# Performance work log

Measured on AMD Instinct MI355X. Metric: run time of the kernel, lower is better.

## Reference

```python
import jax, jax.numpy as jnp
import numpy as np
from jax import lax

K = 3  # kernel size
CO = 64  # out_channels
CI = 64  # in_channels


def setup_inputs() -> dict:
    key = jax.random.key(0)
    k1, k2, k3, k4, k5 = jax.random.split(key, 5)
    x = jax.random.normal(k1, (16, CI, 128, 128), dtype=jnp.float32)
    w1 = jax.random.normal(k2, (2 * CI, 32), dtype=jnp.float32) * 0.05
    b1 = jax.random.normal(k3, (32,), dtype=jnp.float32) * 0.05
    w2 = jax.random.normal(k4, (32, CO * CI * K * K), dtype=jnp.float32) * 0.05
    b2 = jax.random.normal(k5, (CO * CI * K * K,), dtype=jnp.float32) * 0.05
    return {"x": x, "w1": w1, "b1": b1, "w2": w2, "b2": b2}


def reference(x, w1, b1, w2, b2):
    B = x.shape[0]
    # per-sample channel statistics over spatial dims (torch.std is unbiased, ddof=1)
    mean = jnp.mean(x, axis=(2, 3))                      # [B, CI]
    std = jnp.std(x, axis=(2, 3), ddof=1)                # [B, CI]
    stats = jnp.concatenate([mean, std], axis=-1)        # [B, 2*CI]
    h = jax.nn.relu(stats @ w1 + b1)                     # [B, 32]
    kernels = (h @ w2 + b2).reshape(B, CO, CI, K, K)     # per-sample conv kernels

    def conv_one(xi, wi):
        # xi: [CI,H,W], wi: [CO,CI,K,K]; stride=1, padding=1, no bias
        return lax.conv_general_dilated(
            xi[None], wi, window_strides=(1, 1), padding=[(1, 1), (1, 1)],
            dimension_numbers=("NCHW", "OIHW", "NCHW"))[0]

    return jax.vmap(conv_one)(x, kernels)                # [B, CO, H, W]
```

## Files before the change

kernel.cpp:

```cpp
#include <hip/hip_runtime.h>
#include <hip/hip_bf16.h>


#define B_ 16
#define NPIX 16384
#define KEL 36864
#define XT_RS 8320

typedef __attribute__((ext_vector_type(4))) float f32x4;
typedef __attribute__((ext_vector_type(8))) short short8;

static __device__ __forceinline__ short bf16_of(float f) {
    __hip_bfloat16 h = __float2bfloat16(f);
    return *reinterpret_cast<short*>(&h);
}

__global__ __launch_bounds__(256) void xpose_stats(const float* __restrict__ x,
                                                   short* __restrict__ xT,
                                                   float* __restrict__ part) {
    int b = blockIdx.x, cig = blockIdx.y, pt = blockIdx.z;
    int t = threadIdx.x;
    int y = pt * 8 + (t >> 5);
    int x0 = (t & 31) * 4;

    const float* xb = x + ((size_t)(b * 64 + cig * 8)) * NPIX;
    short* xTb = xT + (size_t)b * 128 * XT_RS;

    float s[8], ss[8];
    f32x4 v[8];
    #pragma unroll
    for (int c = 0; c < 8; c++) {
        v[c] = *(const f32x4*)(xb + (size_t)c * NPIX + y * 128 + x0);
        s[c]  = v[c][0] + v[c][1] + v[c][2] + v[c][3];
        ss[c] = v[c][0]*v[c][0] + v[c][1]*v[c][1] + v[c][2]*v[c][2] + v[c][3]*v[c][3];
    }
    #pragma unroll
    for (int xi = 0; xi < 4; xi++) {
        short8 o;
        #pragma unroll
        for (int c = 0; c < 8; c++) o[c] = bf16_of(v[c][xi]);
        *(short8*)(xTb + ((size_t)(y * 130 + x0 + xi + 1)) * 64 + cig * 8) = o;
    }
    if (t < 16) {
        int y2 = pt * 8 + (t & 7);
        int col = (t & 8) ? 129 : 0;
        short8 z = {0, 0, 0, 0, 0, 0, 0, 0};
        *(short8*)(xTb + ((size_t)(y2 * 130 + col)) * 64 + cig * 8) = z;
    }

    __shared__ float red[4][16];
    int lane = t & 63, w = t >> 6;
    #pragma unroll
    for (int c = 0; c < 8; c++) {
        float a = s[c], q = ss[c];
        for (int off = 32; off; off >>= 1) { a += __shfl_down(a, off); q += __shfl_down(q, off); }
        if (lane == 0) { red[w][c * 2] = a; red[w][c * 2 + 1] = q; }
    }
    __syncthreads();
    if (t < 16)
        part[((size_t)((b * 8 + cig) * 16 + pt)) * 16 + t] =
            red[0][t] + red[1][t] + red[2][t] + red[3][t];
}

__global__ __launch_bounds__(256) void kern_gen(const float* __restrict__ part,
                                                const float* __restrict__ w1,
                                                const float* __restrict__ b1,
                                                const float* __restrict__ w2,
                                                const float* __restrict__ b2,
                                                short* __restrict__ wT) {
    __shared__ float st[16][128];
    __shared__ float hT[32][16];
    int t = threadIdx.x;

    for (int id = t; id < 1024; id += 256) {
        int b = id >> 6, ci = id & 63;
        const float* pb = part + ((size_t)((b * 8 + (ci >> 3)) * 16)) * 16 + (ci & 7) * 2;
        float s = 0.f, q = 0.f;
        #pragma unroll
        for (int p = 0; p < 16; p++) { s += pb[p * 16]; q += pb[p * 16 + 1]; }
        float mean = s * (1.f / NPIX);
        float var = fmaxf((q - s * mean) * (1.f / (NPIX - 1)), 0.f);
        st[b][ci] = mean;
        st[b][64 + ci] = sqrtf(var);
    }
    __syncthreads();
    for (int id = t; id < 512; id += 256) {
        int b = id >> 5, jj = id & 31;
        float acc = b1[jj];
        for (int i = 0; i < 128; i++) acc += st[b][i] * w1[i * 32 + jj];
        hT[jj][b] = fmaxf(acc, 0.f);
    }
    __syncthreads();

    int j = blockIdx.x * 256 + t;
    float wv[32];
    #pragma unroll
    for (int i = 0; i < 32; i++) wv[i] = w2[(size_t)i * KEL + j];
    float bv = b2[j];

    float acc[16];
    #pragma unroll
    for (int b = 0; b < 16; b++) acc[b] = bv;
    #pragma unroll
    for (int i = 0; i < 32; i++) {
        float wvi = wv[i];
        const f32x4* hr = (const f32x4*)&hT[i][0];
        #pragma unroll
        for (int q4 = 0; q4 < 4; q4++) {
            f32x4 hq = hr[q4];
            acc[q4 * 4 + 0] += hq[0] * wvi;
            acc[q4 * 4 + 1] += hq[1] * wvi;
            acc[q4 * 4 + 2] += hq[2] * wvi;
            acc[q4 * 4 + 3] += hq[3] * wvi;
        }
    }

    int co = j / 576;
    int rem = j - co * 576;
    int ci = rem / 9;
    int tap = rem - ci * 9;
    size_t dst = (size_t)tap * 4096 + co * 64 + ((((ci >> 3) ^ (co & 7)) << 3) | (ci & 7));
    #pragma unroll
    for (int b = 0; b < 16; b++)
        wT[(size_t)b * KEL + dst] = bf16_of(acc[b]);
}

__global__ __launch_bounds__(512, 1) void conv_mfma(const short* __restrict__ xT,
                                                    const short* __restrict__ wT,
                                                    float* __restrict__ out) {
    __shared__ __align__(16) short xls[10 * 528 * 8];
    __shared__ __align__(16) short wls[9 * 512 * 8];

    int b = blockIdx.x, xt = blockIdx.y, yo = blockIdx.z;
    int x0 = xt * 64, y0 = yo * 8;
    int t = threadIdx.x;
    int l = t & 63, w = t >> 6;
    int xq = w & 3, rh = w >> 2;
    int l15 = l & 15, lg = l >> 4;

    const short* xTb = xT + (size_t)b * 128 * XT_RS;
    const short* wTb = wT + (size_t)b * KEL;

    #pragma unroll
    for (int it = 0; it < 9; it++) {
        int e = it * 512 + t;
        __builtin_amdgcn_global_load_lds(
            (const __attribute__((address_space(1))) void*)(wTb + (size_t)e * 8),
            (__attribute__((address_space(3))) void*)(wls + (it * 512 + (t & ~63)) * 8),
            16, 0, 0);
    }
    #pragma unroll
    for (int lr = 0; lr < 10; lr++) {
        int y = y0 - 1 + lr;
        if (y < 0 || y > 127) {
            short8 z8 = {0, 0, 0, 0, 0, 0, 0, 0};
            for (int e = t; e < 528; e += 512)
                *(short8*)(xls + (lr * 528 + e) * 8) = z8;
        } else {
            #pragma unroll
            for (int it = 0; it < 2; it++) {
                int e = it * 512 + t;
                if (e < 528) {
                    int xi = e >> 3, s = e & 7;
                    const short* src = xTb + (size_t)y * XT_RS
                        + (x0 + xi) * 64 + ((s ^ (xi & 7)) << 3);
                    __builtin_amdgcn_global_load_lds(
                        (const __attribute__((address_space(1))) void*)src,
                        (__attribute__((address_space(3))) void*)
                            (xls + (lr * 528 + it * 512 + (t & ~63)) * 8),
                        16, 0, 0);
                }
            }
        }
    }
    asm volatile("s_waitcnt vmcnt(0) lgkmcnt(0)" ::: "memory");
    __builtin_amdgcn_s_barrier();
    __builtin_amdgcn_sched_barrier(0);

    f32x4 acc[4][4];
    #pragma unroll
    for (int r = 0; r < 4; r++)
        #pragma unroll
        for (int g = 0; g < 4; g++) acc[r][g] = (f32x4){0.f, 0.f, 0.f, 0.f};

    #pragma unroll
    for (int kp = 0; kp < 2; kp++) {
        int sig = kp * 4 + lg;
        int pa = sig ^ (l15 & 7);
        #pragma unroll
        for (int tap = 0; tap < 9; tap++) {
            const int dy = tap / 3, dx = tap % 3;
            short8 a[4], bf[4];
            #pragma unroll
            for (int g = 0; g < 4; g++)
                a[g] = *(const short8*)&wls[(tap * 512 + (g * 16 + l15) * 8 + pa) * 8];
            int xi = xq * 16 + l15 + dx;
            int sw = sig ^ (xi & 7);
            #pragma unroll
            for (int r = 0; r < 4; r++)
                bf[r] = *(const short8*)&xls[((rh * 4 + r + dy) * 528 + xi * 8 + sw) * 8];
            #pragma unroll
            for (int r = 0; r < 4; r++)
                #pragma unroll
                for (int g = 0; g < 4; g++)
                    acc[r][g] = __builtin_amdgcn_mfma_f32_16x16x32_bf16(a[g], bf[r], acc[r][g], 0, 0, 0);
        }
    }

    #pragma unroll
    for (int g = 0; g < 4; g++) {
        float* ob = out + ((size_t)(b * 64 + g * 16 + lg * 4)) * NPIX
                        + (y0 + rh * 4) * 128 + x0 + xq * 16 + l15;
        #pragma unroll
        for (int reg = 0; reg < 4; reg++)
            #pragma unroll
            for (int r = 0; r < 4; r++)
                ob[(size_t)reg * NPIX + r * 128] = acc[r][g][reg];
    }
}

extern "C" void kernel_launch(void* const* d_in, const int* in_sizes, int n_in,
                              void* d_out, int out_size, void* d_ws, size_t ws_size,
                              hipStream_t stream) {
    const float* x  = (const float*)d_in[0];
    const float* w1 = (const float*)d_in[1];
    const float* b1 = (const float*)d_in[2];
    const float* w2 = (const float*)d_in[3];
    const float* b2 = (const float*)d_in[4];
    float* out = (float*)d_out;

    float* part = (float*)d_ws;
    short* wT = (short*)((char*)d_ws + 131072);
    short* xT = (short*)((char*)d_ws + 131072 + 1179648);

    xpose_stats<<<dim3(B_, 8, 16), 256, 0, stream>>>(x, xT, part);
    kern_gen<<<dim3(144), 256, 0, stream>>>(part, w1, b1, w2, b2, wT);
    conv_mfma<<<dim3(B_, 2, 16), 512, 0, stream>>>(xT, wT, out);
}
```

Baseline: 66.40 us.

## Keep conv weights in registers and shrink row tile to raise occupancy

Measured after the change: 115.0 us. +73.1%, slower.

```diff
diff --git a/kernel.cpp b/kernel.cpp
--- a/kernel.cpp
+++ b/kernel.cpp
@@ -119,103 +119,111 @@
     int rem = j - co * 576;
     int ci = rem / 9;
     int tap = rem - ci * 9;
-    size_t dst = (size_t)tap * 4096 + co * 64 + ((((ci >> 3) ^ (co & 7)) << 3) | (ci & 7));
+    size_t dst = (size_t)co * 576 + tap * 64 + ci;
     #pragma unroll
     for (int b = 0; b < 16; b++)
         wT[(size_t)b * KEL + dst] = bf16_of(acc[b]);
 }
 
-__global__ __launch_bounds__(512, 1) void conv_mfma(const short* __restrict__ xT,
-                                                    const short* __restrict__ wT,
-                                                    float* __restrict__ out) {
-    __shared__ __align__(16) short xls[10 * 528 * 8];
-    __shared__ __align__(16) short wls[9 * 512 * 8];
-
-    int b = blockIdx.x, xt = blockIdx.y, yo = blockIdx.z;
-    int x0 = xt * 64, y0 = yo * 8;
+__global__ __attribute__((amdgpu_flat_work_group_size(512, 512),
+                          amdgpu_waves_per_eu(4, 4)))
+void conv_mfma(const short* __restrict__ xT,
+               const short* __restrict__ wT,
+               float* __restrict__ out) {
+    __shared__ __align__(16) short xls[6 * 528 * 8];
+
+    int b = blockIdx.x, xt = blockIdx.y, yt = blockIdx.z;
+    int x0 = xt * 64, y0 = yt * 4;
     int t = threadIdx.x;
     int l = t & 63, w = t >> 6;
-    int xq = w & 3, rh = w >> 2;
+    int cog = w & 3, rh = w >> 2;
     int l15 = l & 15, lg = l >> 4;
 
     const short* xTb = xT + (size_t)b * 128 * XT_RS;
-    const short* wTb = wT + (size_t)b * KEL;
-
-    #pragma unroll
-    for (int it = 0; it < 9; it++) {
+
+    const short* wl = wT + (size_t)b * KEL + (cog * 16 + l15) * 576 + lg * 8;
+    short8 wf0[9], wf1[9];
+    #pragma unroll
+    for (int tap = 0; tap < 9; tap++) {
+        wf0[tap] = *(const short8*)(wl + tap * 64);
+        wf1[tap] = *(const short8*)(wl + tap * 64 + 32);
+    }
+
+    if (yt == 0) {
+        short8 z8 = {0, 0, 0, 0, 0, 0, 0, 0};
+        for (int e = t; e < 528; e += 512) *(short8*)&xls[e * 8] = z8;
+    }
+    if (yt == 31) {
+        short8 z8 = {0, 0, 0, 0, 0, 0, 0, 0};
+        for (int e = t; e < 528; e += 512) *(short8*)&xls[(5 * 528 + e) * 8] = z8;
+    }
+
+    #pragma unroll
+    for (int it = 0; it < 7; it++) {
         int e = it * 512 + t;
-        __builtin_amdgcn_global_load_lds(
-            (const __attribute__((address_space(1))) void*)(wTb + (size_t)e * 8),
-            (__attribute__((address_space(3))) void*)(wls + (it * 512 + (t & ~63)) * 8),
-            16, 0, 0);
-    }
-    #pragma unroll
-    for (int lr = 0; lr < 10; lr++) {
-        int y = y0 - 1 + lr;
-        if (y < 0 || y > 127) {
-            short8 z8 = {0, 0, 0, 0, 0, 0, 0, 0};
-            for (int e = t; e < 528; e += 512)
-                *(short8*)(xls + (lr * 528 + e) * 8) = z8;
-        } else {
+        if (e < 3168) {
+            int lr = e / 528;
+            int rem = e - lr * 528;
+            int xi = rem >> 3, s = rem & 7;
+            int y = y0 - 1 + lr;
+            if ((unsigned)y < 128u) {
+                const short* src = xTb + (size_t)y * XT_RS
+                    + (x0 + xi) * 64 + ((s ^ (xi & 7)) << 3);
+                __builtin_amdgcn_global_load_lds(
+                    (const __attribute__((address_space(1))) void*)src,
+                    (__attribute__((address_space(3))) void*)
+                        (xls + (it * 512 + (t & ~63)) * 8),
+                    16, 0, 0);
+            }
+        }
+    }
+
+    #pragma unroll
+    for (int tap = 0; tap < 9; tap++) {
+        asm volatile("" : "+v"(wf0[tap]));
+        asm volatile("" : "+v"(wf1[tap]));
+    }
+
+    asm volatile("s_waitcnt vmcnt(0) lgkmcnt(0)" ::: "memory");
+    __builtin_amdgcn_s_barrier();
+
+    f32x4 acc[2][4];
+    #pragma unroll
+    for (int r = 0; r < 2; r++)
+        #pragma unroll
+        for (int n = 0; n < 4; n++) acc[r][n] = (f32x4){0.f, 0.f, 0.f, 0.f};
+
+    __builtin_amdgcn_s_setprio(1);
+    #pragma unroll
+    for (int kp = 0; kp < 2; kp++) {
+        int sig = kp * 4 + lg;
+        #pragma unroll
+        for (int tap = 0; tap < 9; tap++) {
+            const int dy = tap / 3, dx = tap % 3;
+            short8 a = kp ? wf1[tap] : wf0[tap];
             #pragma unroll
-            for (int it = 0; it < 2; it++) {
-                int e = it * 512 + t;
-                if (e < 528) {
-                    int xi = e >> 3, s = e & 7;
-                    const short* src = xTb + (size_t)y * XT_RS
-                        + (x0 + xi) * 64 + ((s ^ (xi & 7)) << 3);
-                    __builtin_amdgcn_global_load_lds(
-                        (const __attribute__((address_space(1))) void*)src,
-                        (__attribute__((address_space(3))) void*)
-                            (xls + (lr * 528 + it * 512 + (t & ~63)) * 8),
-                        16, 0, 0);
+            for (int r = 0; r < 2; r++) {
+                int lr = rh * 2 + r + dy;
+                #pragma unroll
+                for (int n = 0; n < 4; n++) {
+                    int xi = n * 16 + l15 + dx;
+                    short8 bf = *(const short8*)&xls[(lr * 528 + xi * 8 + (sig ^ (xi & 7))) * 8];
+                    acc[r][n] = __builtin_amdgcn_mfma_f32_16x16x32_bf16(a, bf, acc[r][n], 0, 0, 0);
                 }
             }
         }
     }
-    asm volatile("s_waitcnt vmcnt(0) lgkmcnt(0)" ::: "memory");
-    __builtin_amdgcn_s_barrier();
-    __builtin_amdgcn_sched_barrier(0);
-
-    f32x4 acc[4][4];
-    #pragma unroll
-    for (int r = 0; r < 4; r++)
-        #pragma unroll
-        for (int g = 0; g < 4; g++) acc[r][g] = (f32x4){0.f, 0.f, 0.f, 0.f};
-
-    #pragma unroll
-    for (int kp = 0; kp < 2; kp++) {
-        int sig = kp * 4 + lg;
-        int pa = sig ^ (l15 & 7);
-        #pragma unroll
-        for (int tap = 0; tap < 9; tap++) {
-            const int dy = tap / 3, dx = tap % 3;
-            short8 a[4], bf[4];
+    __builtin_amdgcn_s_setprio(0);
+
+    #pragma unroll
+    for (int reg = 0; reg < 4; reg++) {
+        float* ob = out + ((size_t)(b * 64 + cog * 16 + lg * 4 + reg)) * NPIX
+                        + (y0 + rh * 2) * 128 + x0 + l15;
+        #pragma unroll
+        for (int r = 0; r < 2; r++)
             #pragma unroll
-            for (int g = 0; g < 4; g++)
-                a[g] = *(const short8*)&wls[(tap * 512 + (g * 16 + l15) * 8 + pa) * 8];
-            int xi = xq * 16 + l15 + dx;
-            int sw = sig ^ (xi & 7);
-            #pragma unroll
-            for (int r = 0; r < 4; r++)
-                bf[r] = *(const short8*)&xls[((rh * 4 + r + dy) * 528 + xi * 8 + sw) * 8];
-            #pragma unroll
-            for (int r = 0; r < 4; r++)
-                #pragma unroll
-                for (int g = 0; g < 4; g++)
-                    acc[r][g] = __builtin_amdgcn_mfma_f32_16x16x32_bf16(a[g], bf[r], acc[r][g], 0, 0, 0);
-        }
-    }
-
-    #pragma unroll
-    for (int g = 0; g < 4; g++) {
-        float* ob = out + ((size_t)(b * 64 + g * 16 + lg * 4)) * NPIX
-                        + (y0 + rh * 4) * 128 + x0 + xq * 16 + l15;
-        #pragma unroll
-        for (int reg = 0; reg < 4; reg++)
-            #pragma unroll
-            for (int r = 0; r < 4; r++)
-                ob[(size_t)reg * NPIX + r * 128] = acc[r][g][reg];
+            for (int n = 0; n < 4; n++)
+                ob[r * 128 + n * 16] = acc[r][n][reg];
     }
 }
 
@@ -235,5 +243,5 @@
 
     xpose_stats<<<dim3(B_, 8, 16), 256, 0, stream>>>(x, xT, part);
     kern_gen<<<dim3(144), 256, 0, stream>>>(part, w1, b1, w2, b2, wT);
-    conv_mfma<<<dim3(B_, 2, 16), 512, 0, stream>>>(xT, wT, out);
-}
+    conv_mfma<<<dim3(B_, 2, 32), 512, 0, stream>>>(xT, wT, out);
+}
```

## Shrink conv tiles and split output channels; halve per-thread batch in kern_gen

Applied to the files above, without the earlier changes.

Measured after the change: 65.82 us. About the same (-0.9%).

```diff
diff --git a/kernel.cpp b/kernel.cpp
--- a/kernel.cpp
+++ b/kernel.cpp
@@ -92,21 +92,22 @@
     }
     __syncthreads();
 
-    int j = blockIdx.x * 256 + t;
+    int j = blockIdx.x * 128 + (t & 127);
+    int bh = t >> 7;
     float wv[32];
     #pragma unroll
     for (int i = 0; i < 32; i++) wv[i] = w2[(size_t)i * KEL + j];
     float bv = b2[j];
 
-    float acc[16];
-    #pragma unroll
-    for (int b = 0; b < 16; b++) acc[b] = bv;
+    float acc[8];
+    #pragma unroll
+    for (int k = 0; k < 8; k++) acc[k] = bv;
     #pragma unroll
     for (int i = 0; i < 32; i++) {
         float wvi = wv[i];
-        const f32x4* hr = (const f32x4*)&hT[i][0];
-        #pragma unroll
-        for (int q4 = 0; q4 < 4; q4++) {
+        const f32x4* hr = (const f32x4*)&hT[i][bh * 8];
+        #pragma unroll
+        for (int q4 = 0; q4 < 2; q4++) {
             f32x4 hq = hr[q4];
             acc[q4 * 4 + 0] += hq[0] * wvi;
             acc[q4 * 4 + 1] += hq[1] * wvi;
@@ -121,32 +122,33 @@
     int tap = rem - ci * 9;
     size_t dst = (size_t)tap * 4096 + co * 64 + ((((ci >> 3) ^ (co & 7)) << 3) | (ci & 7));
     #pragma unroll
-    for (int b = 0; b < 16; b++)
-        wT[(size_t)b * KEL + dst] = bf16_of(acc[b]);
-}
-
-__global__ __launch_bounds__(512, 1) void conv_mfma(const short* __restrict__ xT,
+    for (int k = 0; k < 8; k++)
+        wT[(size_t)(bh * 8 + k) * KEL + dst] = bf16_of(acc[k]);
+}
+
+__global__ __launch_bounds__(256, 2) void conv_mfma(const short* __restrict__ xT,
                                                     const short* __restrict__ wT,
                                                     float* __restrict__ out) {
-    __shared__ __align__(16) short xls[10 * 528 * 8];
-    __shared__ __align__(16) short wls[9 * 512 * 8];
-
-    int b = blockIdx.x, xt = blockIdx.y, yo = blockIdx.z;
-    int x0 = xt * 64, y0 = yo * 8;
+    __shared__ __align__(16) short xls[10 * 272 * 8];
+    __shared__ __align__(16) short wls[9 * 256 * 8];
+
+    int b = blockIdx.x;
+    int xt = blockIdx.y & 3, cog = blockIdx.y >> 2;
+    int ys = blockIdx.z;
+    int x0 = xt * 32, y0 = ys * 8;
     int t = threadIdx.x;
     int l = t & 63, w = t >> 6;
-    int xq = w & 3, rh = w >> 2;
+    int xq = w & 1, rh = w >> 1;
     int l15 = l & 15, lg = l >> 4;
 
     const short* xTb = xT + (size_t)b * 128 * XT_RS;
-    const short* wTb = wT + (size_t)b * KEL;
+    const short* wTb = wT + (size_t)b * KEL + cog * 2048;
 
     #pragma unroll
     for (int it = 0; it < 9; it++) {
-        int e = it * 512 + t;
         __builtin_amdgcn_global_load_lds(
-            (const __attribute__((address_space(1))) void*)(wTb + (size_t)e * 8),
-            (__attribute__((address_space(3))) void*)(wls + (it * 512 + (t & ~63)) * 8),
+            (const __attribute__((address_space(1))) void*)(wTb + (size_t)it * 4096 + t * 8),
+            (__attribute__((address_space(3))) void*)(wls + (it * 256 + (t & ~63)) * 8),
             16, 0, 0);
     }
     #pragma unroll
@@ -154,34 +156,36 @@
         int y = y0 - 1 + lr;
         if (y < 0 || y > 127) {
             short8 z8 = {0, 0, 0, 0, 0, 0, 0, 0};
-            for (int e = t; e < 528; e += 512)
-                *(short8*)(xls + (lr * 528 + e) * 8) = z8;
+            #pragma unroll
+            for (int it = 0; it < 2; it++) {
+                int e = it * 256 + t;
+                if (e < 272) *(short8*)(xls + (lr * 272 + e) * 8) = z8;
+            }
         } else {
             #pragma unroll
             for (int it = 0; it < 2; it++) {
-                int e = it * 512 + t;
-                if (e < 528) {
+                int e = it * 256 + t;
+                if (e < 272) {
                     int xi = e >> 3, s = e & 7;
                     const short* src = xTb + (size_t)y * XT_RS
                         + (x0 + xi) * 64 + ((s ^ (xi & 7)) << 3);
                     __builtin_amdgcn_global_load_lds(
                         (const __attribute__((address_space(1))) void*)src,
                         (__attribute__((address_space(3))) void*)
-                            (xls + (lr * 528 + it * 512 + (t & ~63)) * 8),
+                            (xls + (lr * 272 + it * 256 + (t & ~63)) * 8),
                         16, 0, 0);
                 }
             }
         }
     }
-    asm volatile("s_waitcnt vmcnt(0) lgkmcnt(0)" ::: "memory");
-    __builtin_amdgcn_s_barrier();
-    __builtin_amdgcn_sched_barrier(0);
-
-    f32x4 acc[4][4];
-    #pragma unroll
-    for (int r = 0; r < 4; r++)
-        #pragma unroll
-        for (int g = 0; g < 4; g++) acc[r][g] = (f32x4){0.f, 0.f, 0.f, 0.f};
+    asm volatile("s_waitcnt vmcnt(0)" ::: "memory");
+    __syncthreads();
+
+    f32x4 acc[2][4];
+    #pragma unroll
+    for (int f = 0; f < 2; f++)
+        #pragma unroll
+        for (int r = 0; r < 4; r++) acc[f][r] = (f32x4){0.f, 0.f, 0.f, 0.f};
 
     #pragma unroll
     for (int kp = 0; kp < 2; kp++) {
@@ -190,32 +194,30 @@
         #pragma unroll
         for (int tap = 0; tap < 9; tap++) {
             const int dy = tap / 3, dx = tap % 3;
-            short8 a[4], bf[4];
-            #pragma unroll
-            for (int g = 0; g < 4; g++)
-                a[g] = *(const short8*)&wls[(tap * 512 + (g * 16 + l15) * 8 + pa) * 8];
+            short8 a0 = *(const short8*)&wls[(tap * 256 + l15 * 8 + pa) * 8];
+            short8 a1 = *(const short8*)&wls[(tap * 256 + (16 + l15) * 8 + pa) * 8];
             int xi = xq * 16 + l15 + dx;
             int sw = sig ^ (xi & 7);
             #pragma unroll
+            for (int r = 0; r < 4; r++) {
+                int row = rh * 4 + r + dy;
+                short8 bf = *(const short8*)&xls[(row * 272 + xi * 8 + sw) * 8];
+                acc[0][r] = __builtin_amdgcn_mfma_f32_16x16x32_bf16(a0, bf, acc[0][r], 0, 0, 0);
+                acc[1][r] = __builtin_amdgcn_mfma_f32_16x16x32_bf16(a1, bf, acc[1][r], 0, 0, 0);
+            }
+        }
+    }
+
+    #pragma unroll
+    for (int f = 0; f < 2; f++) {
+        #pragma unroll
+        for (int reg = 0; reg < 4; reg++) {
+            float* ob = out + ((size_t)(b * 64 + cog * 32 + f * 16 + lg * 4 + reg)) * NPIX
+                            + (y0 + rh * 4) * 128 + x0 + xq * 16 + l15;
+            #pragma unroll
             for (int r = 0; r < 4; r++)
-                bf[r] = *(const short8*)&xls[((rh * 4 + r + dy) * 528 + xi * 8 + sw) * 8];
-            #pragma unroll
-            for (int r = 0; r < 4; r++)
-                #pragma unroll
-                for (int g = 0; g < 4; g++)
-                    acc[r][g] = __builtin_amdgcn_mfma_f32_16x16x32_bf16(a[g], bf[r], acc[r][g], 0, 0, 0);
-        }
-    }
-
-    #pragma unroll
-    for (int g = 0; g < 4; g++) {
-        float* ob = out + ((size_t)(b * 64 + g * 16 + lg * 4)) * NPIX
-                        + (y0 + rh * 4) * 128 + x0 + xq * 16 + l15;
-        #pragma unroll
-        for (int reg = 0; reg < 4; reg++)
-            #pragma unroll
-            for (int r = 0; r < 4; r++)
-                ob[(size_t)reg * NPIX + r * 128] = acc[r][g][reg];
+                ob[r * 128] = acc[f][r][reg];
+        }
     }
 }
 
@@ -234,6 +236,6 @@
     short* xT = (short*)((char*)d_ws + 131072 + 1179648);
 
     xpose_stats<<<dim3(B_, 8, 16), 256, 0, stream>>>(x, xT, part);
-    kern_gen<<<dim3(144), 256, 0, stream>>>(part, w1, b1, w2, b2, wT);
-    conv_mfma<<<dim3(B_, 2, 16), 512, 0, stream>>>(xT, wT, out);
-}
+    kern_gen<<<dim3(288), 256, 0, stream>>>(part, w1, b1, w2, b2, wT);
+    conv_mfma<<<dim3(B_, 8, 16), 256, 0, stream>>>(xT, wT, out);
+}
```

## Load conv input fragments directly from global, drop input LDS staging

Applied to the files above, without the earlier changes.

New measurement: 66.46 us. No clear change (+0.1%).

```diff
diff --git a/kernel.cpp b/kernel.cpp
--- a/kernel.cpp
+++ b/kernel.cpp
@@ -25,6 +25,7 @@
 
     const float* xb = x + ((size_t)(b * 64 + cig * 8)) * NPIX;
     short* xTb = xT + (size_t)b * 128 * XT_RS;
+    int kp = cig >> 2, c32 = (cig & 3) * 8;
 
     float s[8], ss[8];
     f32x4 v[8];
@@ -39,13 +40,13 @@
         short8 o;
         #pragma unroll
         for (int c = 0; c < 8; c++) o[c] = bf16_of(v[c][xi]);
-        *(short8*)(xTb + ((size_t)(y * 130 + x0 + xi + 1)) * 64 + cig * 8) = o;
+        *(short8*)(xTb + ((size_t)(y * 260 + kp * 130 + x0 + xi + 1)) * 32 + c32) = o;
     }
     if (t < 16) {
         int y2 = pt * 8 + (t & 7);
         int col = (t & 8) ? 129 : 0;
         short8 z = {0, 0, 0, 0, 0, 0, 0, 0};
-        *(short8*)(xTb + ((size_t)(y2 * 130 + col)) * 64 + cig * 8) = z;
+        *(short8*)(xTb + ((size_t)(y2 * 260 + kp * 130 + col)) * 32 + c32) = z;
     }
 
     __shared__ float red[4][16];
@@ -92,21 +93,22 @@
     }
     __syncthreads();
 
-    int j = blockIdx.x * 256 + t;
+    int j = blockIdx.x * 128 + (t & 127);
+    int bh = t >> 7;
     float wv[32];
     #pragma unroll
     for (int i = 0; i < 32; i++) wv[i] = w2[(size_t)i * KEL + j];
     float bv = b2[j];
 
-    float acc[16];
-    #pragma unroll
-    for (int b = 0; b < 16; b++) acc[b] = bv;
+    float acc[8];
+    #pragma unroll
+    for (int k = 0; k < 8; k++) acc[k] = bv;
     #pragma unroll
     for (int i = 0; i < 32; i++) {
         float wvi = wv[i];
-        const f32x4* hr = (const f32x4*)&hT[i][0];
-        #pragma unroll
-        for (int q4 = 0; q4 < 4; q4++) {
+        const f32x4* hr = (const f32x4*)&hT[i][bh * 8];
+        #pragma unroll
+        for (int q4 = 0; q4 < 2; q4++) {
             f32x4 hq = hr[q4];
             acc[q4 * 4 + 0] += hq[0] * wvi;
             acc[q4 * 4 + 1] += hq[1] * wvi;
@@ -121,14 +123,13 @@
     int tap = rem - ci * 9;
     size_t dst = (size_t)tap * 4096 + co * 64 + ((((ci >> 3) ^ (co & 7)) << 3) | (ci & 7));
     #pragma unroll
-    for (int b = 0; b < 16; b++)
-        wT[(size_t)b * KEL + dst] = bf16_of(acc[b]);
-}
-
-__global__ __launch_bounds__(512, 1) void conv_mfma(const short* __restrict__ xT,
+    for (int k = 0; k < 8; k++)
+        wT[(size_t)(bh * 8 + k) * KEL + dst] = bf16_of(acc[k]);
+}
+
+__global__ __launch_bounds__(512, 4) void conv_mfma(const short* __restrict__ xT,
                                                     const short* __restrict__ wT,
                                                     float* __restrict__ out) {
-    __shared__ __align__(16) short xls[10 * 528 * 8];
     __shared__ __align__(16) short wls[9 * 512 * 8];
 
     int b = blockIdx.x, xt = blockIdx.y, yo = blockIdx.z;
@@ -143,74 +144,57 @@
 
     #pragma unroll
     for (int it = 0; it < 9; it++) {
-        int e = it * 512 + t;
         __builtin_amdgcn_global_load_lds(
-            (const __attribute__((address_space(1))) void*)(wTb + (size_t)e * 8),
+            (const __attribute__((address_space(1))) void*)(wTb + (size_t)(it * 512 + t) * 8),
             (__attribute__((address_space(3))) void*)(wls + (it * 512 + (t & ~63)) * 8),
             16, 0, 0);
     }
-    #pragma unroll
-    for (int lr = 0; lr < 10; lr++) {
-        int y = y0 - 1 + lr;
-        if (y < 0 || y > 127) {
-            short8 z8 = {0, 0, 0, 0, 0, 0, 0, 0};
-            for (int e = t; e < 528; e += 512)
-                *(short8*)(xls + (lr * 528 + e) * 8) = z8;
-        } else {
+    asm volatile("s_waitcnt vmcnt(0)" ::: "memory");
+    __syncthreads();
+
+    int px = x0 + xq * 16 + l15;
+    int yb = y0 + rh * 4;
+
+    f32x4 acc[4][4];
+    #pragma unroll
+    for (int r = 0; r < 4; r++)
+        #pragma unroll
+        for (int g = 0; g < 4; g++) acc[r][g] = (f32x4){0.f, 0.f, 0.f, 0.f};
+
+    #pragma unroll
+    for (int kp = 0; kp < 2; kp++) {
+        int pa = (kp * 4 + lg) ^ (l15 & 7);
+        #pragma unroll
+        for (int dx = 0; dx < 3; dx++) {
+            short8 bf6[6];
             #pragma unroll
-            for (int it = 0; it < 2; it++) {
-                int e = it * 512 + t;
-                if (e < 528) {
-                    int xi = e >> 3, s = e & 7;
-                    const short* src = xTb + (size_t)y * XT_RS
-                        + (x0 + xi) * 64 + ((s ^ (xi & 7)) << 3);
-                    __builtin_amdgcn_global_load_lds(
-                        (const __attribute__((address_space(1))) void*)src,
-                        (__attribute__((address_space(3))) void*)
-                            (xls + (lr * 528 + it * 512 + (t & ~63)) * 8),
-                        16, 0, 0);
-                }
+            for (int s = 0; s < 6; s++) {
+                int yin = yb - 1 + s;
+                short8 v = {0, 0, 0, 0, 0, 0, 0, 0};
+                if ((unsigned)yin < 128u)
+                    v = *(const short8*)(xTb + (size_t)yin * XT_RS
+                            + (size_t)(kp * 130 + px + dx) * 32 + lg * 8);
+                bf6[s] = v;
+            }
+            #pragma unroll
+            for (int dy = 0; dy < 3; dy++) {
+                int tap = dy * 3 + dx;
+                short8 a[4];
+                #pragma unroll
+                for (int g = 0; g < 4; g++)
+                    a[g] = *(const short8*)&wls[(tap * 512 + (g * 16 + l15) * 8 + pa) * 8];
+                #pragma unroll
+                for (int r = 0; r < 4; r++)
+                    #pragma unroll
+                    for (int g = 0; g < 4; g++)
+                        acc[r][g] = __builtin_amdgcn_mfma_f32_16x16x32_bf16(a[g], bf6[r + dy], acc[r][g], 0, 0, 0);
             }
         }
     }
-    asm volatile("s_waitcnt vmcnt(0) lgkmcnt(0)" ::: "memory");
-    __builtin_amdgcn_s_barrier();
-    __builtin_amdgcn_sched_barrier(0);
-
-    f32x4 acc[4][4];
-    #pragma unroll
-    for (int r = 0; r < 4; r++)
-        #pragma unroll
-        for (int g = 0; g < 4; g++) acc[r][g] = (f32x4){0.f, 0.f, 0.f, 0.f};
-
-    #pragma unroll
-    for (int kp = 0; kp < 2; kp++) {
-        int sig = kp * 4 + lg;
-        int pa = sig ^ (l15 & 7);
-        #pragma unroll
-        for (int tap = 0; tap < 9; tap++) {
-            const int dy = tap / 3, dx = tap % 3;
-            short8 a[4], bf[4];
-            #pragma unroll
-            for (int g = 0; g < 4; g++)
-                a[g] = *(const short8*)&wls[(tap * 512 + (g * 16 + l15) * 8 + pa) * 8];
-            int xi = xq * 16 + l15 + dx;
-            int sw = sig ^ (xi & 7);
-            #pragma unroll
-            for (int r = 0; r < 4; r++)
-                bf[r] = *(const short8*)&xls[((rh * 4 + r + dy) * 528 + xi * 8 + sw) * 8];
-            #pragma unroll
-            for (int r = 0; r < 4; r++)
-                #pragma unroll
-                for (int g = 0; g < 4; g++)
-                    acc[r][g] = __builtin_amdgcn_mfma_f32_16x16x32_bf16(a[g], bf[r], acc[r][g], 0, 0, 0);
-        }
-    }
 
     #pragma unroll
     for (int g = 0; g < 4; g++) {
-        float* ob = out + ((size_t)(b * 64 + g * 16 + lg * 4)) * NPIX
-                        + (y0 + rh * 4) * 128 + x0 + xq * 16 + l15;
+        float* ob = out + ((size_t)(b * 64 + g * 16 + lg * 4)) * NPIX + yb * 128 + px;
         #pragma unroll
         for (int reg = 0; reg < 4; reg++)
             #pragma unroll
@@ -234,6 +218,6 @@
     short* xT = (short*)((char*)d_ws + 131072 + 1179648);
 
     xpose_stats<<<dim3(B_, 8, 16), 256, 0, stream>>>(x, xT, part);
-    kern_gen<<<dim3(144), 256, 0, stream>>>(part, w1, b1, w2, b2, wT);
+    kern_gen<<<dim3(288), 256, 0, stream>>>(part, w1, b1, w2, b2, wT);
     conv_mfma<<<dim3(B_, 2, 16), 512, 0, stream>>>(xT, wT, out);
 }
```
